# Performance work log

Hardware: AMD Instinct MI355X
Metric: run time of the kernel (lower is better)

Reference implementation:

```python
import jax, jax.numpy as jnp
import numpy as np

DIM = 1024
NUM_HEADS = 16
HEAD_DIM = DIM // NUM_HEADS
TOKENS_PER_FRAME = 1560


def setup_inputs() -> dict:
    key = jax.random.key(0)
    ks = jax.random.split(key, 10)
    B, T = 2, 16
    N = T * TOKENS_PER_FRAME
    s = 1.0 / np.sqrt(DIM)
    return {
        "x": jax.random.normal(ks[0], (B, N, DIM), dtype=jnp.float32),
        "c": jax.random.normal(ks[1], (B, T, DIM), dtype=jnp.float32),
        "Wq": jax.random.normal(ks[2], (DIM, DIM), dtype=jnp.float32) * s,
        "bq": jnp.zeros((DIM,), dtype=jnp.float32),
        "Wk": jax.random.normal(ks[3], (DIM, DIM), dtype=jnp.float32) * s,
        "bk": jnp.zeros((DIM,), dtype=jnp.float32),
        "Wv": jax.random.normal(ks[4], (DIM, DIM), dtype=jnp.float32) * s,
        "bv": jnp.zeros((DIM,), dtype=jnp.float32),
        "Wo": jax.random.normal(ks[5], (DIM, DIM), dtype=jnp.float32) * s,
        "bo": jnp.zeros((DIM,), dtype=jnp.float32),
    }


def reference(x, c, Wq, bq, Wk, bk, Wv, bv, Wo, bo):
    B, N, dim = x.shape
    T = c.shape[1]
    tpf = N // T
    H, hd = NUM_HEADS, HEAD_DIM
    scale = hd ** (-0.5)

    q = x @ Wq.T + bq            # [B, N, dim]
    k = c @ Wk.T + bk            # [B, T, dim]
    v = c @ Wv.T + bv            # [B, T, dim]

    qh = q.reshape(B, T, tpf, H, hd)
    kh = k.reshape(B, T, 1, H, hd)
    vh = v.reshape(B, T, 1, H, hd)

    # per-frame cross-attention with kv_len=1: scores [B,T,tpf,H,1]
    scores = (qh * kh).sum(-1, keepdims=True) * scale
    attn = jax.nn.softmax(scores, axis=-1)   # softmax over length-1 kv axis == 1.0
    out = attn * vh                          # broadcast v: [B,T,tpf,H,hd]

    out = out.reshape(B, N, dim)
    return out @ Wo.T + bo
```

## Files before the change

### kernel.cpp

```cpp
#include <hip/hip_runtime.h>
#include <hip/hip_bf16.h>


#define DIM   1024
#define K4    (DIM / 4)
#define MROWS 32
#define TPF   1560
#define CHUNK 26
#define SPLITS 60

typedef float fvec4 __attribute__((ext_vector_type(4)));

__global__ __launch_bounds__(256) void gemm32(const float* __restrict__ A,
                                              const float* __restrict__ W,
                                              const float* __restrict__ bias,
                                              float* __restrict__ C) {
    __shared__ fvec4 aS[MROWS * 64];

    const int tid  = threadIdx.x;
    const int wave = tid >> 6;
    const int lane = tid & 63;
    const int j    = blockIdx.x * 4 + wave;

    const fvec4* __restrict__ A4   = (const fvec4*)A;
    const fvec4* __restrict__ Wrow = (const fvec4*)(W + (size_t)j * DIM);

    float acc[MROWS];
#pragma unroll
    for (int r = 0; r < MROWS; ++r) acc[r] = 0.f;

    for (int kt = 0; kt < 4; ++kt) {
#pragma unroll
        for (int i = tid; i < MROWS * 64; i += 256) {
            int r  = i >> 6;
            int c4 = i & 63;
            aS[i] = A4[r * K4 + kt * 64 + c4];
        }
        __syncthreads();

        fvec4 w = Wrow[kt * 64 + lane];
#pragma unroll
        for (int r = 0; r < MROWS; ++r) {
            fvec4 a = aS[r * 64 + lane];
            acc[r] += w.x * a.x + w.y * a.y + w.z * a.z + w.w * a.w;
        }
        __syncthreads();
    }

#pragma unroll
    for (int r = 0; r < MROWS; ++r) {
        float v = acc[r];
        for (int off = 32; off > 0; off >>= 1) v += __shfl_down(v, off, 64);
        acc[r] = v;
    }

    if (lane == 0) {
        const float b = bias[j];
#pragma unroll
        for (int r = 0; r < MROWS; ++r) C[r * DIM + j] = acc[r] + b;
    }
}

__global__ __launch_bounds__(256) void bcast(const float* __restrict__ y,
                                             float* __restrict__ out) {
    const int bt = blockIdx.x / SPLITS;
    const int ch = blockIdx.x % SPLITS;

    const fvec4 val = ((const fvec4*)(y + (size_t)bt * DIM))[threadIdx.x];

    fvec4* o = (fvec4*)out + ((size_t)bt * TPF + (size_t)ch * CHUNK) * K4;
#pragma unroll
    for (int i = 0; i < CHUNK; ++i) {
        __builtin_nontemporal_store(val, &o[(size_t)i * K4 + threadIdx.x]);
    }
}

extern "C" void kernel_launch(void* const* d_in, const int* in_sizes, int n_in,
                              void* d_out, int out_size, void* d_ws, size_t ws_size,
                              hipStream_t stream) {
    const float* c  = (const float*)d_in[1];
    const float* Wv = (const float*)d_in[6];
    const float* bv = (const float*)d_in[7];
    const float* Wo = (const float*)d_in[8];
    const float* bo = (const float*)d_in[9];
    float* out = (float*)d_out;

    float* v = (float*)d_ws;
    float* y = (float*)d_ws + MROWS * DIM;

    gemm32<<<256, 256, 0, stream>>>(c, Wv, bv, v);
    gemm32<<<256, 256, 0, stream>>>(v, Wo, bo, y);
    bcast<<<MROWS * SPLITS, 256, 0, stream>>>(y, out);
}
```

Before: 345.1 us.

## Rework thin GEMM to register-held weights and halve broadcast chunk size

The thin GEMM drops its shared-memory staging and syncthreads. Each block now computes two output columns, with each wave handling 8 rows and the weights held in registers, over 512 blocks. The broadcast kernel doubles its block count with half-size chunks and replaces nontemporal stores with plain stores. The total is dominated by the roughly 200MB broadcast write, so the GEMM changes only trim small launches, and plain stores may pollute the cache.

```diff
diff --git a/kernel.cpp b/kernel.cpp
--- a/kernel.cpp
+++ b/kernel.cpp
@@ -2,62 +2,68 @@
 #include <hip/hip_bf16.h>
 
 
-#define DIM   1024
-#define K4    (DIM / 4)
-#define MROWS 32
-#define TPF   1560
-#define CHUNK 26
-#define SPLITS 60
+#define DIM    1024
+#define K4     (DIM / 4)
+#define MROWS  32
+#define TPF    1560
+#define CHUNK  13
+#define SPLITS 120
 
 typedef float fvec4 __attribute__((ext_vector_type(4)));
 
-__global__ __launch_bounds__(256) void gemm32(const float* __restrict__ A,
-                                              const float* __restrict__ W,
-                                              const float* __restrict__ bias,
-                                              float* __restrict__ C) {
-    __shared__ fvec4 aS[MROWS * 64];
+__global__ __launch_bounds__(256) void gemm_thin(const float* __restrict__ A,
+                                                 const float* __restrict__ W,
+                                                 const float* __restrict__ bias,
+                                                 float* __restrict__ C) {
+    const int wave = threadIdx.x >> 6;
+    const int lane = threadIdx.x & 63;
+    const int j0   = blockIdx.x * 2;
+    const int r0   = wave * 8;
 
-    const int tid  = threadIdx.x;
-    const int wave = tid >> 6;
-    const int lane = tid & 63;
-    const int j    = blockIdx.x * 4 + wave;
+    const fvec4* __restrict__ A4 = (const fvec4*)A;
+    const fvec4* __restrict__ W0 = (const fvec4*)(W + (size_t)j0 * DIM);
+    const fvec4* __restrict__ W1 = (const fvec4*)(W + (size_t)(j0 + 1) * DIM);
 
-    const fvec4* __restrict__ A4   = (const fvec4*)A;
-    const fvec4* __restrict__ Wrow = (const fvec4*)(W + (size_t)j * DIM);
+    fvec4 wa[4], wb[4];
+#pragma unroll
+    for (int t = 0; t < 4; ++t) {
+        wa[t] = W0[t * 64 + lane];
+        wb[t] = W1[t * 64 + lane];
+    }
 
-    float acc[MROWS];
+    float accA[8], accB[8];
 #pragma unroll
-    for (int r = 0; r < MROWS; ++r) acc[r] = 0.f;
+    for (int r = 0; r < 8; ++r) { accA[r] = 0.f; accB[r] = 0.f; }
 
-    for (int kt = 0; kt < 4; ++kt) {
 #pragma unroll
-        for (int i = tid; i < MROWS * 64; i += 256) {
-            int r  = i >> 6;
-            int c4 = i & 63;
-            aS[i] = A4[r * K4 + kt * 64 + c4];
+    for (int r = 0; r < 8; ++r) {
+        const fvec4* __restrict__ Ar = A4 + (size_t)(r0 + r) * K4;
+#pragma unroll
+        for (int t = 0; t < 4; ++t) {
+            fvec4 a = Ar[t * 64 + lane];
+            accA[r] += a.x * wa[t].x + a.y * wa[t].y + a.z * wa[t].z + a.w * wa[t].w;
+            accB[r] += a.x * wb[t].x + a.y * wb[t].y + a.z * wb[t].z + a.w * wb[t].w;
         }
-        __syncthreads();
-
-        fvec4 w = Wrow[kt * 64 + lane];
-#pragma unroll
-        for (int r = 0; r < MROWS; ++r) {
-            fvec4 a = aS[r * 64 + lane];
-            acc[r] += w.x * a.x + w.y * a.y + w.z * a.z + w.w * a.w;
-        }
-        __syncthreads();
     }
 
 #pragma unroll
-    for (int r = 0; r < MROWS; ++r) {
-        float v = acc[r];
-        for (int off = 32; off > 0; off >>= 1) v += __shfl_down(v, off, 64);
-        acc[r] = v;
+    for (int r = 0; r < 8; ++r) {
+        float va = accA[r], vb = accB[r];
+#pragma unroll
+        for (int off = 32; off > 0; off >>= 1) {
+            va += __shfl_down(va, off, 64);
+            vb += __shfl_down(vb, off, 64);
+        }
+        accA[r] = va; accB[r] = vb;
     }
 
     if (lane == 0) {
-        const float b = bias[j];
+        const float b0 = bias[j0], b1 = bias[j0 + 1];
 #pragma unroll
-        for (int r = 0; r < MROWS; ++r) C[r * DIM + j] = acc[r] + b;
+        for (int r = 0; r < 8; ++r) {
+            C[(size_t)(r0 + r) * DIM + j0]     = accA[r] + b0;
+            C[(size_t)(r0 + r) * DIM + j0 + 1] = accB[r] + b1;
+        }
     }
 }
 
@@ -71,7 +77,7 @@
     fvec4* o = (fvec4*)out + ((size_t)bt * TPF + (size_t)ch * CHUNK) * K4;
 #pragma unroll
     for (int i = 0; i < CHUNK; ++i) {
-        __builtin_nontemporal_store(val, &o[(size_t)i * K4 + threadIdx.x]);
+        o[(size_t)i * K4 + threadIdx.x] = val;
     }
 }
 
@@ -88,7 +94,7 @@
     float* v = (float*)d_ws;
     float* y = (float*)d_ws + MROWS * DIM;
 
-    gemm32<<<256, 256, 0, stream>>>(c, Wv, bv, v);
-    gemm32<<<256, 256, 0, stream>>>(v, Wo, bo, y);
+    gemm_thin<<<DIM / 2, 256, 0, stream>>>(c, Wv, bv, v);
+    gemm_thin<<<DIM / 2, 256, 0, stream>>>(v, Wo, bo, y);
     bcast<<<MROWS * SPLITS, 256, 0, stream>>>(y, out);
 }
```

New measurement: 330.3 us. 4.3% less time.
